# Performance work log

Hardware: AMD Instinct MI355X
Metric: run time of the kernel (lower is better)

The kernel has to match this reference:

```python
import jax, jax.numpy as jnp
import numpy as np

N = 3072
FEAT = 128
E = 24576


def setup_inputs() -> dict:
    key = jax.random.key(0)
    k1, k2, k3, k4 = jax.random.split(key, 4)
    x = jax.random.normal(k1, (N, FEAT), dtype=jnp.float32)
    edge_index = jax.random.randint(k2, (2, E), 0, N, dtype=jnp.int32)
    batch = jnp.zeros((N,), dtype=jnp.int32)
    # lin: Linear(2*FEAT, 1)
    w = jax.random.normal(k3, (2 * FEAT,), dtype=jnp.float32) / np.sqrt(2 * FEAT)
    b = jax.random.normal(k4, (), dtype=jnp.float32) * 0.01
    return {"x": x, "edge_index": edge_index, "batch": batch, "w": w, "b": b}


def _cc_labels(adj):
    """Connected-component labels via min-label propagation + pointer jumping.
    Labels equal the minimum node index of each component, so ranking them by
    value reproduces scipy's first-occurrence component ordering."""
    n = adj.shape[0]
    adj = jax.lax.stop_gradient(adj)

    def body(state):
        labels, _ = state
        neigh = jnp.where(adj > 0, labels[None, :], n).min(axis=1)  # [n]
        new = jnp.minimum(labels, neigh)
        new = jnp.minimum(new, new[new])  # pointer jumping
        return new, jnp.any(new != labels)

    labels, _ = jax.lax.while_loop(lambda s: s[1], body,
                                   (jnp.arange(n), jnp.array(True)))
    return labels


def reference(x, edge_index, batch, w, b):
    n, f = x.shape
    idx = jnp.arange(n)
    src, dst = edge_index[0], edge_index[1]
    # undirected: duplicate each edge in both directions (coalesce in the
    # original dedups; dense scatter-set below is equivalent since duplicate
    # (u,v) edges get identical scores)
    s2 = jnp.concatenate([src, dst])
    d2 = jnp.concatenate([dst, src])
    # per-edge raw score: lin(concat(x[u], x[v]))  ->  tanh
    e = jnp.tanh(x[s2] @ w[:f] + x[d2] @ w[f:] + b)  # [2E]

    zero = jnp.zeros((n, n), dtype=x.dtype)
    A = zero.at[s2, d2].set(1.0).at[idx, idx].set(0.0)   # self-loops removed
    S = zero.at[s2, d2].set(e).at[idx, idx].set(0.0)
    contract = (e > 0.0).astype(x.dtype)                 # tanh -> threshold 0
    A_c = zero.at[s2, d2].max(contract).at[idx, idx].set(0.0)

    labels = _cc_labels(A_c)                             # min-node-index labels
    roots = (labels == idx).astype(jnp.int32)
    cluster = (jnp.cumsum(roots) - 1)[labels]            # consecutive 0..K-1
    C = jax.nn.one_hot(cluster, n, dtype=x.dtype)        # [n, n] (padded to n)

    single = (A_c.sum(axis=1) + A_c.sum(axis=0)) == 0    # isolated under contraction
    S = S.at[idx, idx].set(single.astype(x.dtype))

    X_new = (S @ C).T @ x                                # [n(padK), f]
    A_new = (C.T @ A @ C).at[idx, idx].set(0.0)          # dense coarsened adjacency
    new_batch = jnp.zeros((n,), dtype=batch.dtype).at[cluster].max(batch)
    return X_new, A_new, new_batch, cluster
```

## Files before the change

kernel.cpp:

```cpp
#include <hip/hip_runtime.h>
#include <math.h>

#define N 3072
#define FEAT 128
#define NE 24576
#define NP (2 * NE)
#define DOUT_ZB 9606
#define WS_ZB 294
#define PSTRIDE 64
#define EPT 24

__device__ __forceinline__ void wave_agg_add(bool valid, int key, float val,
                                             float* base, int stride, int off) {
    int lane = threadIdx.x & 63;
    unsigned long long active = __ballot(valid ? 1 : 0);
    while (active) {
        int leader = __ffsll(active) - 1;
        int lkey = __shfl(key, leader);
        bool mine = valid && (key == lkey);
        unsigned long long grp = __ballot(mine ? 1 : 0);
        float v = mine ? val : 0.0f;
        #pragma unroll
        for (int o = 32; o; o >>= 1) v += __shfl_xor(v, o);
        if (lane == leader)
            atomicAdd(&base[(size_t)lkey * stride + off], v);
        active &= ~grp;
    }
}

__global__ void k_dots_zero(const float* __restrict__ x, const float* __restrict__ w,
                            float* __restrict__ a, float* __restrict__ c,
                            float4* __restrict__ zout, float4* __restrict__ zws) {
    int b = blockIdx.x;
    int l = threadIdx.x;
    if (b < N) {
        const float* xi = x + b * FEAT;
        float pa = xi[l] * w[l] + xi[l + 64] * w[l + 64];
        float pc = xi[l] * w[FEAT + l] + xi[l + 64] * w[FEAT + l + 64];
        for (int off = 32; off; off >>= 1) {
            pa += __shfl_down(pa, off);
            pc += __shfl_down(pc, off);
        }
        if (l == 0) { a[b] = pa; c[b] = pc; }
    } else {
        float4 z = {0.f, 0.f, 0.f, 0.f};
        float4* dst;
        size_t base;
        if (b < N + DOUT_ZB) { base = (size_t)(b - N) * 256; dst = zout; }
        else                 { base = (size_t)(b - N - DOUT_ZB) * 256; dst = zws; }
        dst[base + l]       = z;
        dst[base + 64 + l]  = z;
        dst[base + 128 + l] = z;
        dst[base + 192 + l] = z;
    }
}

__global__ void k_edge_pairs(const int* __restrict__ ei, const float* __restrict__ a,
                             const float* __restrict__ c, const float* __restrict__ bb,
                             unsigned* __restrict__ ep, int* __restrict__ notsingle,
                             unsigned* __restrict__ mask, int* __restrict__ pcnt,
                             unsigned long long* __restrict__ ptab) {
    int t = blockIdx.x * blockDim.x + threadIdx.x;
    if (t >= NE) return;
    int u = ei[t], v = ei[NE + t];
    unsigned wpk = (unsigned)u | ((unsigned)v << 12);
    if (u != v) {
        float b = bb[0];
        float su = a[u] + c[v] + b;
        float sv = a[v] + c[u] + b;
        unsigned fu = (su > 0.f) ? 1u : 0u;
        unsigned fv = (sv > 0.f) ? 1u : 0u;
        wpk |= (fu << 24) | (fv << 25);
        if (fu | fv) { notsingle[u] = 1; notsingle[v] = 1; }
        unsigned pos = (unsigned)u * N + (unsigned)v;
        unsigned bit = 1u << (pos & 31u);
        unsigned old = atomicOr(&mask[pos >> 5], bit);
        if (!(old & bit)) {
            wpk |= (1u << 26);
            float e = tanhf(su);
            int sl = atomicAdd(&pcnt[v], 1);
            if (sl < PSTRIDE)
                ptab[(size_t)v * PSTRIDE + sl] =
                    ((unsigned long long)__float_as_uint(e) << 32) | (unsigned)u;
        }
        pos = (unsigned)v * N + (unsigned)u;
        bit = 1u << (pos & 31u);
        old = atomicOr(&mask[pos >> 5], bit);
        if (!(old & bit)) {
            wpk |= (1u << 27);
            float e = tanhf(sv);
            int sl = atomicAdd(&pcnt[u], 1);
            if (sl < PSTRIDE)
                ptab[(size_t)u * PSTRIDE + sl] =
                    ((unsigned long long)__float_as_uint(e) << 32) | (unsigned)v;
        }
    }
    ep[t] = wpk;
}

__global__ void __launch_bounds__(1024)
k_prop_gather(const unsigned* __restrict__ ep, const float* __restrict__ x,
              const int* __restrict__ pcnt, const unsigned long long* __restrict__ ptab,
              const int* __restrict__ notsingle, float* __restrict__ y,
              int* __restrict__ cluster, float* __restrict__ out_cluster) {
    __shared__ int lab[N];
    __shared__ int ssum[1024];
    __shared__ unsigned short rk[N];
    __shared__ int flag;
    if (blockIdx.x == 0) {
        int t = threadIdx.x;
        unsigned er[EPT];
        #pragma unroll
        for (int j = 0; j < EPT; ++j) er[j] = ep[t + j * 1024];
        for (int i = t; i < N; i += 1024) lab[i] = i;
        for (;;) {
            __syncthreads();
            if (t == 0) flag = 0;
            __syncthreads();
            #pragma unroll
            for (int j = 0; j < EPT; ++j) {
                unsigned wpk = er[j];
                int u = wpk & 0xFFF, v = (wpk >> 12) & 0xFFF;
                if (wpk & (1u << 24)) {
                    int lv = lab[v];
                    if (lv < lab[u]) { atomicMin(&lab[u], lv); flag = 1; }
                }
                if (wpk & (1u << 25)) {
                    int lu = lab[u];
                    if (lu < lab[v]) { atomicMin(&lab[v], lu); flag = 1; }
                }
            }
            for (int i = t; i < N; i += 1024) {
                int m = lab[i];
                int mm = lab[m];
                while (mm < m) { m = mm; mm = lab[m]; }
                if (m < lab[i]) { atomicMin(&lab[i], m); flag = 1; }
            }
            __syncthreads();
            if (!flag) break;
        }
        int i0 = 3 * t;
        int r0 = (lab[i0] == i0);
        int r1 = (lab[i0 + 1] == i0 + 1);
        int r2 = (lab[i0 + 2] == i0 + 2);
        int s = r0 + r1 + r2;
        ssum[t] = s;
        __syncthreads();
        for (int off = 1; off < 1024; off <<= 1) {
            int val = (t >= off) ? ssum[t - off] : 0;
            __syncthreads();
            ssum[t] += val;
            __syncthreads();
        }
        int run = ssum[t] - s;
        run += r0; rk[i0]     = (unsigned short)(run - 1);
        run += r1; rk[i0 + 1] = (unsigned short)(run - 1);
        run += r2; rk[i0 + 2] = (unsigned short)(run - 1);
        __syncthreads();
        for (int j = t; j < N; j += 1024) {
            int cl = rk[lab[j]];
            cluster[j] = cl;
            out_cluster[j] = (float)cl;
        }
    } else {
        int q = (blockIdx.x - 1) * 16 + (threadIdx.x >> 6);
        int lane = threadIdx.x & 63;
        int cnt = pcnt[q]; if (cnt > PSTRIDE) cnt = PSTRIDE;
        const unsigned long long* row = ptab + (size_t)q * PSTRIDE;
        float acc0 = 0.f, acc1 = 0.f;
        for (int j = 0; j < cnt; ++j) {
            unsigned long long s = row[j];
            int p = (int)(s & 0xFFFFFFFFu);
            float e = __uint_as_float((unsigned)(s >> 32));
            const float* xp = x + p * FEAT;
            acc0 += e * xp[lane];
            acc1 += e * xp[lane + 64];
        }
        if (!notsingle[q]) {
            const float* xq = x + q * FEAT;
            acc0 += xq[lane];
            acc1 += xq[lane + 64];
        }
        float* yq = y + q * FEAT;
        yq[lane] = acc0;
        yq[lane + 64] = acc1;
    }
}

__global__ void k_reduce_anew(const float* __restrict__ y, const int* __restrict__ cluster,
                              const unsigned* __restrict__ ep,
                              float* __restrict__ Xnew, float* __restrict__ Anew) {
    int gid = blockIdx.x * blockDim.x + threadIdx.x;
    int wid = gid >> 6, lane = gid & 63;
    if (wid < 6144) {
        int f = wid & (FEAT - 1);
        int chunk = wid >> 7;
        int q = chunk * 64 + lane;
        wave_agg_add(true, cluster[q], y[q * FEAT + f], Xnew, FEAT, f);
    } else {
        int s = (wid - 6144) * 64 + lane;
        unsigned wpk = ep[s];
        int u = wpk & 0xFFF, v = (wpk >> 12) & 0xFFF;
        int cu = cluster[u], cv = cluster[v];
        bool o0 = ((wpk & (1u << 26)) != 0) && (cu != cv);
        bool o1 = ((wpk & (1u << 27)) != 0) && (cu != cv);
        wave_agg_add(o0, cu * N + cv, 1.0f, Anew, 1, 0);
        wave_agg_add(o1, cv * N + cu, 1.0f, Anew, 1, 0);
    }
}

extern "C" void kernel_launch(void* const* d_in, const int* in_sizes, int n_in,
                              void* d_out, int out_size, void* d_ws, size_t ws_size,
                              hipStream_t stream) {
    const float* x  = (const float*)d_in[0];
    const int*   ei = (const int*)d_in[1];
    const float* w  = (const float*)d_in[3];
    const float* bb = (const float*)d_in[4];

    char* ws = (char*)d_ws;
    size_t off = 0;
    unsigned* mask = (unsigned*)(ws + off); off += (size_t)N * N / 8;
    int* pcnt      = (int*)(ws + off);      off += (size_t)N * 4;
    int* notsing   = (int*)(ws + off);      off += (size_t)N * 4;
    float* a       = (float*)(ws + off);    off += (size_t)N * 4;
    float* c       = (float*)(ws + off);    off += (size_t)N * 4;
    int* cluster   = (int*)(ws + off);      off += (size_t)N * 4;
    unsigned* ep   = (unsigned*)(ws + off); off += (size_t)NE * 4;
    float* y       = (float*)(ws + off);    off += (size_t)N * FEAT * 4;
    unsigned long long* ptab = (unsigned long long*)(ws + off); off += (size_t)N * PSTRIDE * 8;

    float* Xnew        = (float*)d_out;
    float* Anew        = Xnew + (size_t)N * FEAT;
    float* out_cluster = Anew + (size_t)N * N + N;

    k_dots_zero<<<N + DOUT_ZB + WS_ZB, 64, 0, stream>>>(x, w, a, c,
                                                        (float4*)d_out, (float4*)ws);
    k_edge_pairs<<<NE / 256, 256, 0, stream>>>(ei, a, c, bb, ep, notsing,
                                               mask, pcnt, ptab);
    k_prop_gather<<<1 + N / 16, 1024, 0, stream>>>(ep, x, pcnt, ptab, notsing, y,
                                                   cluster, out_cluster);
    k_reduce_anew<<<(6528 * 64) / 256, 256, 0, stream>>>(y, cluster, ep, Xnew, Anew);
}
```

Before: 140.1 us.

## Fuse edge, propagation and reduction kernels into one persistent kernel with grid barriers

Merges the edge-pair, label-propagation/gather and reduction kernels into a single 256-block persistent kernel separated by software grid barriers. This removes kernel launch gaps. It also replaces the N*N/8-byte dedup bitmask, and the atomicOr calls that filled it, with per-row duplicate detection over ptab entries, recorded in a per-node ballot mask. The zero-fill kernel uses larger blocks and no longer clears the large bitmask. The cost is a spin-based grid barrier that assumes all 256 blocks are co-resident, and an O(cnt^2) shared-memory duplicate scan per row.

```diff
diff --git a/kernel.cpp b/kernel.cpp
--- a/kernel.cpp
+++ b/kernel.cpp
@@ -4,11 +4,14 @@
 #define N 3072
 #define FEAT 128
 #define NE 24576
-#define NP (2 * NE)
-#define DOUT_ZB 9606
-#define WS_ZB 294
 #define PSTRIDE 64
 #define EPT 24
+#define NBLK 256
+#define DOTB 768
+#define OUTZ4 2459136
+#define OUTZB 2402
+#define WSZ4 1540
+#define WSZB 2
 
 __device__ __forceinline__ void wave_agg_add(bool valid, int key, float val,
                                              float* base, int stride, int off) {
@@ -28,87 +31,107 @@
     }
 }
 
-__global__ void k_dots_zero(const float* __restrict__ x, const float* __restrict__ w,
-                            float* __restrict__ a, float* __restrict__ c,
-                            float4* __restrict__ zout, float4* __restrict__ zws) {
-    int b = blockIdx.x;
-    int l = threadIdx.x;
-    if (b < N) {
-        const float* xi = x + b * FEAT;
-        float pa = xi[l] * w[l] + xi[l + 64] * w[l + 64];
-        float pc = xi[l] * w[FEAT + l] + xi[l + 64] * w[FEAT + l + 64];
+__device__ __forceinline__ void gsync(int* bar, int* lgen) {
+    __syncthreads();
+    if (threadIdx.x == 0) {
+        __threadfence();
+        int g = ++(*lgen);
+        if (atomicAdd(&bar[0], 1) == (int)gridDim.x - 1) {
+            __hip_atomic_store(&bar[0], 0, __ATOMIC_RELAXED, __HIP_MEMORY_SCOPE_AGENT);
+            __threadfence();
+            atomicAdd(&bar[1], 1);
+        } else {
+            while (__hip_atomic_load(&bar[1], __ATOMIC_RELAXED,
+                                     __HIP_MEMORY_SCOPE_AGENT) < g)
+                __builtin_amdgcn_s_sleep(8);
+        }
+        __threadfence();
+    } else {
+        ++(*lgen);
+    }
+    __syncthreads();
+}
+
+__global__ void k_init(const float* __restrict__ x, const float* __restrict__ w,
+                       float* __restrict__ a, float* __restrict__ c,
+                       float4* __restrict__ zout, float4* __restrict__ zws) {
+    int b = blockIdx.x, t = threadIdx.x;
+    if (b < DOTB) {
+        int node = b * 4 + (t >> 6);
+        int lane = t & 63;
+        const float* xi = x + node * FEAT;
+        float pa = xi[lane] * w[lane] + xi[lane + 64] * w[lane + 64];
+        float pc = xi[lane] * w[FEAT + lane] + xi[lane + 64] * w[FEAT + lane + 64];
         for (int off = 32; off; off >>= 1) {
             pa += __shfl_down(pa, off);
             pc += __shfl_down(pc, off);
         }
-        if (l == 0) { a[b] = pa; c[b] = pc; }
+        if (lane == 0) { a[node] = pa; c[node] = pc; }
+    } else if (b < DOTB + OUTZB) {
+        float4 z = {0.f, 0.f, 0.f, 0.f};
+        int base = (b - DOTB) * 1024;
+        #pragma unroll
+        for (int k = 0; k < 4; ++k) {
+            int idx = base + k * 256 + t;
+            if (idx < OUTZ4) zout[idx] = z;
+        }
     } else {
         float4 z = {0.f, 0.f, 0.f, 0.f};
-        float4* dst;
-        size_t base;
-        if (b < N + DOUT_ZB) { base = (size_t)(b - N) * 256; dst = zout; }
-        else                 { base = (size_t)(b - N - DOUT_ZB) * 256; dst = zws; }
-        dst[base + l]       = z;
-        dst[base + 64 + l]  = z;
-        dst[base + 128 + l] = z;
-        dst[base + 192 + l] = z;
-    }
-}
-
-__global__ void k_edge_pairs(const int* __restrict__ ei, const float* __restrict__ a,
-                             const float* __restrict__ c, const float* __restrict__ bb,
-                             unsigned* __restrict__ ep, int* __restrict__ notsingle,
-                             unsigned* __restrict__ mask, int* __restrict__ pcnt,
-                             unsigned long long* __restrict__ ptab) {
-    int t = blockIdx.x * blockDim.x + threadIdx.x;
-    if (t >= NE) return;
-    int u = ei[t], v = ei[NE + t];
-    unsigned wpk = (unsigned)u | ((unsigned)v << 12);
-    if (u != v) {
-        float b = bb[0];
-        float su = a[u] + c[v] + b;
-        float sv = a[v] + c[u] + b;
-        unsigned fu = (su > 0.f) ? 1u : 0u;
-        unsigned fv = (sv > 0.f) ? 1u : 0u;
-        wpk |= (fu << 24) | (fv << 25);
-        if (fu | fv) { notsingle[u] = 1; notsingle[v] = 1; }
-        unsigned pos = (unsigned)u * N + (unsigned)v;
-        unsigned bit = 1u << (pos & 31u);
-        unsigned old = atomicOr(&mask[pos >> 5], bit);
-        if (!(old & bit)) {
-            wpk |= (1u << 26);
-            float e = tanhf(su);
+        int base = (b - DOTB - OUTZB) * 1024;
+        #pragma unroll
+        for (int k = 0; k < 4; ++k) {
+            int idx = base + k * 256 + t;
+            if (idx < WSZ4) zws[idx] = z;
+        }
+    }
+}
+
+__global__ void __launch_bounds__(1024, 4)
+k_mega(const int* __restrict__ ei, const float* __restrict__ x,
+       const float* __restrict__ a, const float* __restrict__ c,
+       const float* __restrict__ bb, int* __restrict__ bar,
+       int* __restrict__ pcnt, int* __restrict__ notsingle,
+       unsigned* __restrict__ ep, unsigned long long* __restrict__ qmask,
+       float* __restrict__ y, unsigned long long* __restrict__ ptab,
+       int* __restrict__ cluster, float* __restrict__ Xnew,
+       float* __restrict__ Anew, float* __restrict__ out_cluster) {
+    __shared__ int lab[N];
+    __shared__ int ssum[1024];
+    __shared__ unsigned short rk[N];
+    __shared__ int sh_p[16 * 64];
+    __shared__ int flag;
+    int t = threadIdx.x, blk = blockIdx.x;
+    int wv = t >> 6, lane = t & 63;
+    int lgen = 0;
+
+    if (t < 96) {
+        int s = blk * 96 + t;
+        int u = ei[s], v = ei[NE + s];
+        unsigned wpk = (unsigned)u | ((unsigned)v << 12);
+        if (u != v) {
+            float b = bb[0];
+            float su = a[u] + c[v] + b;
+            float sv = a[v] + c[u] + b;
+            unsigned fu = (su > 0.f) ? 1u : 0u;
+            unsigned fv = (sv > 0.f) ? 1u : 0u;
+            wpk |= (fu << 24) | (fv << 25);
+            if (fu | fv) { notsingle[u] = 1; notsingle[v] = 1; }
+            float eu = tanhf(su);
             int sl = atomicAdd(&pcnt[v], 1);
             if (sl < PSTRIDE)
                 ptab[(size_t)v * PSTRIDE + sl] =
-                    ((unsigned long long)__float_as_uint(e) << 32) | (unsigned)u;
-        }
-        pos = (unsigned)v * N + (unsigned)u;
-        bit = 1u << (pos & 31u);
-        old = atomicOr(&mask[pos >> 5], bit);
-        if (!(old & bit)) {
-            wpk |= (1u << 27);
-            float e = tanhf(sv);
-            int sl = atomicAdd(&pcnt[u], 1);
+                    ((unsigned long long)__float_as_uint(eu) << 32) | (unsigned)u;
+            float ev2 = tanhf(sv);
+            sl = atomicAdd(&pcnt[u], 1);
             if (sl < PSTRIDE)
                 ptab[(size_t)u * PSTRIDE + sl] =
-                    ((unsigned long long)__float_as_uint(e) << 32) | (unsigned)v;
-        }
-    }
-    ep[t] = wpk;
-}
-
-__global__ void __launch_bounds__(1024)
-k_prop_gather(const unsigned* __restrict__ ep, const float* __restrict__ x,
-              const int* __restrict__ pcnt, const unsigned long long* __restrict__ ptab,
-              const int* __restrict__ notsingle, float* __restrict__ y,
-              int* __restrict__ cluster, float* __restrict__ out_cluster) {
-    __shared__ int lab[N];
-    __shared__ int ssum[1024];
-    __shared__ unsigned short rk[N];
-    __shared__ int flag;
-    if (blockIdx.x == 0) {
-        int t = threadIdx.x;
+                    ((unsigned long long)__float_as_uint(ev2) << 32) | (unsigned)v;
+        }
+        ep[s] = wpk;
+    }
+    gsync(bar, &lgen);
+
+    if (blk == 0) {
         unsigned er[EPT];
         #pragma unroll
         for (int j = 0; j < EPT; ++j) er[j] = ep[t + j * 1024];
@@ -163,49 +186,63 @@
             out_cluster[j] = (float)cl;
         }
     } else {
-        int q = (blockIdx.x - 1) * 16 + (threadIdx.x >> 6);
-        int lane = threadIdx.x & 63;
-        int cnt = pcnt[q]; if (cnt > PSTRIDE) cnt = PSTRIDE;
-        const unsigned long long* row = ptab + (size_t)q * PSTRIDE;
-        float acc0 = 0.f, acc1 = 0.f;
-        for (int j = 0; j < cnt; ++j) {
-            unsigned long long s = row[j];
-            int p = (int)(s & 0xFFFFFFFFu);
-            float e = __uint_as_float((unsigned)(s >> 32));
-            const float* xp = x + p * FEAT;
-            acc0 += e * xp[lane];
-            acc1 += e * xp[lane + 64];
-        }
-        if (!notsingle[q]) {
-            const float* xq = x + q * FEAT;
-            acc0 += xq[lane];
-            acc1 += xq[lane + 64];
-        }
-        float* yq = y + q * FEAT;
-        yq[lane] = acc0;
-        yq[lane + 64] = acc1;
-    }
-}
-
-__global__ void k_reduce_anew(const float* __restrict__ y, const int* __restrict__ cluster,
-                              const unsigned* __restrict__ ep,
-                              float* __restrict__ Xnew, float* __restrict__ Anew) {
-    int gid = blockIdx.x * blockDim.x + threadIdx.x;
-    int wid = gid >> 6, lane = gid & 63;
-    if (wid < 6144) {
-        int f = wid & (FEAT - 1);
-        int chunk = wid >> 7;
-        int q = chunk * 64 + lane;
-        wave_agg_add(true, cluster[q], y[q * FEAT + f], Xnew, FEAT, f);
-    } else {
-        int s = (wid - 6144) * 64 + lane;
-        unsigned wpk = ep[s];
-        int u = wpk & 0xFFF, v = (wpk >> 12) & 0xFFF;
-        int cu = cluster[u], cv = cluster[v];
-        bool o0 = ((wpk & (1u << 26)) != 0) && (cu != cv);
-        bool o1 = ((wpk & (1u << 27)) != 0) && (cu != cv);
-        wave_agg_add(o0, cu * N + cv, 1.0f, Anew, 1, 0);
-        wave_agg_add(o1, cv * N + cu, 1.0f, Anew, 1, 0);
+        int q = (blk - 1) * 16 + wv;
+        if (q < N) {
+            int cnt = pcnt[q]; if (cnt > PSTRIDE) cnt = PSTRIDE;
+            const unsigned long long* row = ptab + (size_t)q * PSTRIDE;
+            int myp = -1 - lane;
+            float mye = 0.f;
+            if (lane < cnt) {
+                unsigned long long s = row[lane];
+                myp = (int)(s & 0xFFFFFFFFu);
+                mye = __uint_as_float((unsigned)(s >> 32));
+            }
+            sh_p[wv * 64 + lane] = myp;
+            bool dup = false;
+            for (int j = 0; j < lane && !dup; ++j)
+                dup = (sh_p[wv * 64 + j] == myp);
+            bool valid = (lane < cnt) && !dup;
+            unsigned long long m = __ballot(valid ? 1 : 0);
+            if (lane == 0) qmask[q] = m;
+            float acc0 = 0.f, acc1 = 0.f;
+            for (int j = 0; j < cnt; ++j) {
+                if (!((m >> j) & 1ull)) continue;
+                int p = __shfl(myp, j);
+                float e = __shfl(mye, j);
+                const float* xp = x + p * FEAT;
+                acc0 += e * xp[lane];
+                acc1 += e * xp[lane + 64];
+            }
+            if (!notsingle[q]) {
+                const float* xq = x + q * FEAT;
+                acc0 += xq[lane];
+                acc1 += xq[lane + 64];
+            }
+            float* yq = y + q * FEAT;
+            yq[lane] = acc0;
+            yq[lane + 64] = acc1;
+        }
+    }
+    gsync(bar, &lgen);
+
+    for (int gw = blk * 16 + wv; gw < 9216; gw += NBLK * 16) {
+        if (gw < 6144) {
+            int f = gw & (FEAT - 1);
+            int chunk = gw >> 7;
+            int q = chunk * 64 + lane;
+            wave_agg_add(true, cluster[q], y[q * FEAT + f], Xnew, FEAT, f);
+        } else {
+            int q = gw - 6144;
+            int cnt = pcnt[q]; if (cnt > PSTRIDE) cnt = PSTRIDE;
+            unsigned long long m = qmask[q];
+            bool valid = (lane < cnt) && ((m >> lane) & 1ull);
+            int p = 0;
+            if (valid) p = (int)(ptab[(size_t)q * PSTRIDE + lane] & 0xFFFFFFFFu);
+            int cq = cluster[q];
+            int cp = valid ? cluster[p] : 0;
+            valid = valid && (cp != cq);
+            wave_agg_add(valid, cp * N + cq, 1.0f, Anew, 1, 0);
+        }
     }
 }
 
@@ -219,25 +256,24 @@
 
     char* ws = (char*)d_ws;
     size_t off = 0;
-    unsigned* mask = (unsigned*)(ws + off); off += (size_t)N * N / 8;
-    int* pcnt      = (int*)(ws + off);      off += (size_t)N * 4;
-    int* notsing   = (int*)(ws + off);      off += (size_t)N * 4;
-    float* a       = (float*)(ws + off);    off += (size_t)N * 4;
-    float* c       = (float*)(ws + off);    off += (size_t)N * 4;
-    int* cluster   = (int*)(ws + off);      off += (size_t)N * 4;
-    unsigned* ep   = (unsigned*)(ws + off); off += (size_t)NE * 4;
-    float* y       = (float*)(ws + off);    off += (size_t)N * FEAT * 4;
+    int* bar      = (int*)(ws + off);      off += 64;
+    int* pcnt     = (int*)(ws + off);      off += (size_t)N * 4;
+    int* notsing  = (int*)(ws + off);      off += (size_t)N * 4;
+    float* a      = (float*)(ws + off);    off += (size_t)N * 4;
+    float* c      = (float*)(ws + off);    off += (size_t)N * 4;
+    int* cluster  = (int*)(ws + off);      off += (size_t)N * 4;
+    unsigned* ep  = (unsigned*)(ws + off); off += (size_t)NE * 4;
+    unsigned long long* qmask = (unsigned long long*)(ws + off); off += (size_t)N * 8;
+    float* y      = (float*)(ws + off);    off += (size_t)N * FEAT * 4;
     unsigned long long* ptab = (unsigned long long*)(ws + off); off += (size_t)N * PSTRIDE * 8;
 
     float* Xnew        = (float*)d_out;
     float* Anew        = Xnew + (size_t)N * FEAT;
     float* out_cluster = Anew + (size_t)N * N + N;
 
-    k_dots_zero<<<N + DOUT_ZB + WS_ZB, 64, 0, stream>>>(x, w, a, c,
-                                                        (float4*)d_out, (float4*)ws);
-    k_edge_pairs<<<NE / 256, 256, 0, stream>>>(ei, a, c, bb, ep, notsing,
-                                               mask, pcnt, ptab);
-    k_prop_gather<<<1 + N / 16, 1024, 0, stream>>>(ep, x, pcnt, ptab, notsing, y,
-                                                   cluster, out_cluster);
-    k_reduce_anew<<<(6528 * 64) / 256, 256, 0, stream>>>(y, cluster, ep, Xnew, Anew);
-}
+    k_init<<<DOTB + OUTZB + WSZB, 256, 0, stream>>>(x, w, a, c,
+                                                    (float4*)d_out, (float4*)ws);
+    k_mega<<<NBLK, 1024, 0, stream>>>(ei, x, a, c, bb, bar, pcnt, notsing,
+                                      ep, qmask, y, ptab, cluster,
+                                      Xnew, Anew, out_cluster);
+}
```

Result: slower. 161.5 us (+15.2%).
